# Optimization experiments

Hardware: AMD Instinct MI355X
Metric: run time of the kernel (lower is better)

The kernel has to match this reference:

```python
import jax, jax.numpy as jnp
import numpy as np

EPS = 1e-5

def conv1d(x, w, b, stride, pad):
    # x: [N, Cin, L], w: [Cout, Cin, K]
    out = jax.lax.conv_general_dilated(x, w, (stride,), [(pad, pad)], dimension_numbers=('NCH', 'OIH', 'NCH'))
    return out + b[None, :, None]

def bn_eval(x, g, b):
    # BatchNorm1d in eval mode with running_mean=0, running_var=1
    return x * (g / jnp.sqrt(1.0 + EPS))[None, :, None] + b[None, :, None]

def maxpool3(x):
    return jax.lax.reduce_window(x, -jnp.inf, jax.lax.max, (1, 1, 3), (1, 1, 3), 'VALID')

def layer_norm(x, g, b):
    m = x.mean(-1, keepdims=True)
    v = ((x - m) ** 2).mean(-1, keepdims=True)
    return (x - m) / jnp.sqrt(v + EPS) * g + b

def lstm_dir(x, w_ih, w_hh, b_ih, b_hh, reverse):
    # x: [B, S, I]; torch gate order i, f, g, o
    B = x.shape[0]; H = w_hh.shape[1]
    xs = jnp.einsum('bsi,gi->bsg', x, w_ih) + b_ih + b_hh
    if reverse:
        xs = xs[:, ::-1]
    def step(carry, xt):
        h, c = carry
        gates = xt + h @ w_hh.T
        i, f, g, o = jnp.split(gates, 4, axis=-1)
        c = jax.nn.sigmoid(f) * c + jax.nn.sigmoid(i) * jnp.tanh(g)
        h = jax.nn.sigmoid(o) * jnp.tanh(c)
        return (h, c), h
    init = (jnp.zeros((B, H), x.dtype), jnp.zeros((B, H), x.dtype))
    _, hs = jax.lax.scan(step, init, jnp.swapaxes(xs, 0, 1))
    hs = jnp.swapaxes(hs, 0, 1)
    return hs[:, ::-1] if reverse else hs

def setup_inputs() -> dict:
    key = jax.random.key(0)
    ks = iter(jax.random.split(key, 48))
    def rn(shape, s=0.05):
        return jax.random.normal(next(ks), shape, jnp.float32) * s
    B, S, C, T, F0, Hg, Hl, NC = 64, 20, 8, 3000, 64, 128, 256, 5
    return dict(
        x=jax.random.normal(next(ks), (B, S, C, T), jnp.float32),
        edge_index=jax.random.randint(next(ks), (2, 56), 0, C, jnp.int32),
        conv1_w=rn((16, 1, 7)), conv1_b=jnp.zeros(16), bn1_g=jnp.ones(16), bn1_b=jnp.zeros(16),
        conv2_w=rn((32, 16, 5)), conv2_b=jnp.zeros(32), bn2_g=jnp.ones(32), bn2_b=jnp.zeros(32),
        conv3_w=rn((F0, 32, 3)), conv3_b=jnp.zeros(F0), bn3_g=jnp.ones(F0), bn3_b=jnp.zeros(F0),
        gcn0_w=rn((Hg, F0)), gcn0_b=jnp.zeros(Hg),
        gcn1_w=rn((Hg, Hg)), gcn1_b=jnp.zeros(Hg),
        gnn_ln_g=jnp.ones(Hg), gnn_ln_b=jnp.zeros(Hg),
        w_ih_l0=rn((4 * Hl, Hg)), w_hh_l0=rn((4 * Hl, Hl)), b_ih_l0=jnp.zeros(4 * Hl), b_hh_l0=jnp.zeros(4 * Hl),
        w_ih_l0r=rn((4 * Hl, Hg)), w_hh_l0r=rn((4 * Hl, Hl)), b_ih_l0r=jnp.zeros(4 * Hl), b_hh_l0r=jnp.zeros(4 * Hl),
        w_ih_l1=rn((4 * Hl, 2 * Hl)), w_hh_l1=rn((4 * Hl, Hl)), b_ih_l1=jnp.zeros(4 * Hl), b_hh_l1=jnp.zeros(4 * Hl),
        w_ih_l1r=rn((4 * Hl, 2 * Hl)), w_hh_l1r=rn((4 * Hl, Hl)), b_ih_l1r=jnp.zeros(4 * Hl), b_hh_l1r=jnp.zeros(4 * Hl),
        lstm_ln_g=jnp.ones(2 * Hl), lstm_ln_b=jnp.zeros(2 * Hl),
        cls_w=rn((NC, 2 * Hl)), cls_b=jnp.zeros(NC),
    )

def reference(x, edge_index, conv1_w, conv1_b, bn1_g, bn1_b, conv2_w, conv2_b, bn2_g, bn2_b, conv3_w, conv3_b, bn3_g, bn3_b, gcn0_w, gcn0_b, gcn1_w, gcn1_b, gnn_ln_g, gnn_ln_b, w_ih_l0, w_hh_l0, b_ih_l0, b_hh_l0, w_ih_l0r, w_hh_l0r, b_ih_l0r, b_hh_l0r, w_ih_l1, w_hh_l1, b_ih_l1, b_hh_l1, w_ih_l1r, w_hh_l1r, b_ih_l1r, b_hh_l1r, lstm_ln_g, lstm_ln_b, cls_w, cls_b):
    B, S, C, T = x.shape
    # batched per-channel CNN over all B*S epochs at once (original: python double loop)
    h = x.reshape(B * S * C, 1, T)
    h = maxpool3(jax.nn.relu(bn_eval(conv1d(h, conv1_w, conv1_b, 2, 3), bn1_g, bn1_b)))
    h = maxpool3(jax.nn.relu(bn_eval(conv1d(h, conv2_w, conv2_b, 2, 2), bn2_g, bn2_b)))
    h = jax.nn.relu(bn_eval(conv1d(h, conv3_w, conv3_b, 1, 1), bn3_g, bn3_b))
    feats = h.mean(-1).reshape(B * S, C, -1)  # AdaptiveAvgPool1d(1) -> [BS, C, 64]
    # GCNConv normalized adjacency: D^-1/2 (A + I) D^-1/2, graph is tiny (C nodes) so dense is exact and efficient
    src, dst = edge_index[0], edge_index[1]
    A = jnp.zeros((C, C), x.dtype).at[dst, src].add(1.0) + jnp.eye(C, dtype=x.dtype)
    dinv = 1.0 / jnp.sqrt(A.sum(1))
    An = A * dinv[:, None] * dinv[None, :]
    g1 = jax.nn.relu(jnp.einsum('ij,bjf->bif', An, feats @ gcn0_w.T) + gcn0_b)  # dropout off (eval)
    g2 = jnp.einsum('ij,bjf->bif', An, g1 @ gcn1_w.T) + gcn1_b
    g2 = layer_norm(g2, gnn_ln_g, gnn_ln_b)
    emb = g2.mean(1).reshape(B, S, -1)  # mean over nodes -> [B, S, 128]
    l0 = jnp.concatenate([lstm_dir(emb, w_ih_l0, w_hh_l0, b_ih_l0, b_hh_l0, False),
                          lstm_dir(emb, w_ih_l0r, w_hh_l0r, b_ih_l0r, b_hh_l0r, True)], -1)
    l1 = jnp.concatenate([lstm_dir(l0, w_ih_l1, w_hh_l1, b_ih_l1, b_hh_l1, False),
                          lstm_dir(l0, w_ih_l1r, w_hh_l1r, b_ih_l1r, b_hh_l1r, True)], -1)
    out = layer_norm(l1, lstm_ln_g, lstm_ln_b)
    return out @ cls_w.T + cls_b  # [B, S, 5]
```

## Files before the change

kernel.cpp:

```cpp
#include <hip/hip_runtime.h>
#include <hip/hip_bf16.h>

#define DEVI __device__ __forceinline__

typedef _Float16 h2f16 __attribute__((ext_vector_type(2)));
typedef _Float16 f16x4 __attribute__((ext_vector_type(4)));
typedef _Float16 f16x8 __attribute__((ext_vector_type(8)));
typedef float    f32x4 __attribute__((ext_vector_type(4)));
union U4H { uint4 u; h2f16 h[4]; };
union F8  { f16x8 v8; f16x4 v4[2]; };

DEVI float sigf(float x){ return 1.f/(1.f + __expf(-x)); }
DEVI float tanh_f(float x){
  float ax = fabsf(x);
  float e = __expf(-2.f*ax);
  float t = (1.f - e)/(1.f + e);
  return copysignf(t, x);
}
DEVI h2f16 hmax2(h2f16 a, h2f16 b){
  h2f16 r; r[0] = a[0] > b[0] ? a[0] : b[0]; r[1] = a[1] > b[1] ? a[1] : b[1]; return r;
}

__global__ __launch_bounds__(256) void k_prep(
  const int* __restrict__ ei, float* __restrict__ An,
  const float* __restrict__ w2, const float* __restrict__ w3,
  const float* __restrict__ bg2, const float* __restrict__ bg3,
  _Float16* __restrict__ bw2f, _Float16* __restrict__ bw3f,
  const float* __restrict__ a0, const float* __restrict__ a1,
  const float* __restrict__ a2, const float* __restrict__ a3,
  const float* __restrict__ a4, const float* __restrict__ a5,
  _Float16* __restrict__ o0, _Float16* __restrict__ o1,
  _Float16* __restrict__ o2, _Float16* __restrict__ o3,
  _Float16* __restrict__ o4, _Float16* __restrict__ o5,
  const float* __restrict__ whh0, const float* __restrict__ whh0r,
  const float* __restrict__ whh1, const float* __restrict__ whh1r,
  h2f16* __restrict__ wt0f, h2f16* __restrict__ wt0r,
  h2f16* __restrict__ wt1f, h2f16* __restrict__ wt1r)
{
  const int bid = blockIdx.x, tid = threadIdx.x;
  if (bid == 0){
    __shared__ float A[64];
    __shared__ float dinv[8];
    if (tid<64) A[tid] = ((tid>>3)==(tid&7)) ? 1.f : 0.f;
    __syncthreads();
    if (tid==0){
      for (int e=0;e<56;e++){ int s=ei[e], d=ei[56+e]; A[d*8+s] += 1.f; }
    }
    __syncthreads();
    if (tid<8){ float s=0.f; for (int j=0;j<8;j++) s+=A[tid*8+j]; dinv[tid]=rsqrtf(s); }
    __syncthreads();
    if (tid<64) An[tid] = A[tid]*dinv[tid>>3]*dinv[tid&7];
    return;
  }
  if (bid <= 24){
    const int i = (bid-1)*256 + tid;
    const float rs = rsqrtf(1.f+1e-5f);
    if (i < 3072){
      const int j = i&7, m = (i>>3)&15, g = (i>>7)&3, nt = (i>>9)&1, s = i>>10;
      const int kk = 32*s + 8*g + j;
      const int k = kk >> 4, ic = kk & 15, oc = nt*16 + m;
      bw2f[i] = (_Float16)((k < 5 ? w2[oc*80 + ic*5 + k] : 0.f) * (bg2[oc]*rs));
    }
    if (i < 6144){
      const int j = i&7, m = (i>>3)&15, g = (i>>7)&3, wv = (i>>9)&3, s = i>>11;
      const int kk = 32*s + 8*g + j;
      const int k = kk >> 5, ic = kk & 31, oc = wv*16 + m;
      bw3f[i] = (_Float16)(w3[oc*96 + ic*3 + k] * (bg3[oc]*rs));
    }
    return;
  }
  if (bid <= 5240){
    const int i = (bid-25)*256 + tid;
    if      (i <  131072) o0[i] = (_Float16)a0[i];
    else if (i <  262144) o1[i-131072] = (_Float16)a1[i-131072];
    else if (i <  786432) o2[i-262144] = (_Float16)a2[i-262144];
    else if (i < 1310720) o3[i-786432] = (_Float16)a3[i-786432];
    else if (i < 1318912) o4[i-1310720] = (_Float16)a4[i-1310720];
    else if (i < 1335296) o5[i-1318912] = (_Float16)a5[i-1318912];
    return;
  }
  {
    __shared__ float tl[64][65];
    const int t = bid - 5241;
    const int which = t >> 6, tile = t & 63;
    const int tg = tile >> 2, tc = tile & 3;
    const float* in = (which==0) ? whh0 : (which==1) ? whh0r : (which==2) ? whh1 : whh1r;
    h2f16* outp    = (which==0) ? wt0f : (which==1) ? wt0r  : (which==2) ? wt1f : wt1r;
    #pragma unroll
    for (int p=0;p<16;p++){
      const int lin = p*256 + tid;
      const int r = lin >> 6, cc = lin & 63;
      tl[r][cc] = in[(tg*64 + r)*256 + tc*64 + cc];
    }
    __syncthreads();
    #pragma unroll
    for (int p=0;p<8;p++){
      const int lin = p*256 + tid;
      const int gl = lin & 63, jph = lin >> 6;
      h2f16 v;
      v[0] = (_Float16)tl[gl][2*jph];
      v[1] = (_Float16)tl[gl][2*jph+1];
      outp[(long)(tc*32 + jph)*1024 + tg*64 + gl] = v;
    }
  }
}

__global__ __launch_bounds__(512,8) void k_conv(
    const float* __restrict__ x,
    const float* __restrict__ w1g, const float* __restrict__ c1b,
    const float* __restrict__ bg1, const float* __restrict__ bb1,
    const _Float16* __restrict__ bw2f,
    const float* __restrict__ c2b, const float* __restrict__ bg2, const float* __restrict__ bb2,
    const _Float16* __restrict__ bw3f,
    const float* __restrict__ c3b, const float* __restrict__ bg3, const float* __restrict__ bb3,
    _Float16* __restrict__ feats)
{
  __shared__ __align__(16) unsigned char smb[38592];
  __shared__ h2f16 w1p[16][4];
  __shared__ float kb1o[16], kb2o[32], kb3o[64];
  __shared__ float redc[8][16];
  h2f16* sxh = reinterpret_cast<h2f16*>(smb + 20160);
  const int tid = threadIdx.x;
  const long sig = blockIdx.x;
  const float* xg = x + sig*3000;

  {
    const float4* xg4 = reinterpret_cast<const float4*>(xg);
    for (int i=tid; i<750; i+=512){
      float4 v = xg4[i];
      h2f16 p0; p0[0]=(_Float16)v.x; p0[1]=(_Float16)v.y;
      h2f16 p1; p1[0]=(_Float16)v.z; p1[1]=(_Float16)v.w;
      sxh[2*i+2] = p0; sxh[2*i+3] = p1;
    }
    if (tid<3){
      h2f16 z; z[0]=(_Float16)0.f; z[1]=(_Float16)0.f;
      sxh[tid<2 ? tid : 1502] = z;
    }
    if (tid<32){
      const int rr = tid>>3, cp = tid&7;
      const int row = (rr<2) ? rr : (500+rr);
      h2f16 z; z[0]=(_Float16)0.f; z[1]=(_Float16)0.f;
      *reinterpret_cast<h2f16*>(smb + row*40 + 4*cp) = z;
    }
    const float rs = rsqrtf(1.f+1e-5f);
    if (tid<64){
      const int c = tid>>2, j = tid&3;
      const float s = bg1[c]*rs;
      h2f16 p;
      if (j==0){ p[0]=(_Float16)0.f; p[1]=(_Float16)(w1g[c*7+0]*s); }
      else     { p[0]=(_Float16)(w1g[c*7+2*j-1]*s); p[1]=(_Float16)(w1g[c*7+2*j]*s); }
      w1p[c][j] = p;
    }
    if (tid<16) kb1o[tid] = c1b[tid]*(bg1[tid]*rs) + bb1[tid];
    if (tid<32) kb2o[tid] = c2b[tid]*(bg2[tid]*rs) + bb2[tid];
    if (tid<64) kb3o[tid] = c3b[tid]*(bg3[tid]*rs) + bb3[tid];
  }
  __syncthreads();

  {
    const int cp = tid & 7;
    h2f16 wpa[4], wpb[4];
    #pragma unroll
    for (int j=0;j<4;j++){ wpa[j] = w1p[2*cp][j]; wpb[j] = w1p[2*cp+1][j]; }
    const float oa = kb1o[2*cp], ob = kb1o[2*cp+1];
    for (int u = tid>>3; u<500; u+=64){
      h2f16 xq[6];
      #pragma unroll
      for (int r=0;r<6;r++) xq[r] = sxh[3*u + r];
      float a0=0.f,a1=0.f,a2=0.f,b0=0.f,b1=0.f,b2=0.f;
      #pragma unroll
      for (int j=0;j<4;j++){
        a0 = __builtin_amdgcn_fdot2(xq[j],   wpa[j], a0, false);
        a1 = __builtin_amdgcn_fdot2(xq[j+1], wpa[j], a1, false);
        a2 = __builtin_amdgcn_fdot2(xq[j+2], wpa[j], a2, false);
        b0 = __builtin_amdgcn_fdot2(xq[j],   wpb[j], b0, false);
        b1 = __builtin_amdgcn_fdot2(xq[j+1], wpb[j], b1, false);
        b2 = __builtin_amdgcn_fdot2(xq[j+2], wpb[j], b2, false);
      }
      const float ya = fmaxf(fmaxf(fmaxf(a0,a1),a2) + oa, 0.f);
      const float yb = fmaxf(fmaxf(fmaxf(b0,b1),b2) + ob, 0.f);
      h2f16 p; p[0]=(_Float16)ya; p[1]=(_Float16)yb;
      *reinterpret_cast<h2f16*>(smb + (u+2)*40 + 4*cp) = p;
    }
  }
  __syncthreads();

  const int wv = tid >> 6, lane = tid & 63;
  const int m = lane & 15, g = lane >> 4;

  {
    const int nt = wv & 1;
    f16x8 bf[3];
    #pragma unroll
    for (int s=0;s<3;s++)
      bf[s] = *reinterpret_cast<const f16x8*>(&bw2f[(((s*2+nt)*4+g)*16+m)*8]);
    const int oc = nt*16 + m;
    const float of = kb2o[oc];
    #pragma unroll
    for (int i=0;i<4;i++){
      const int mt = (wv>>1) + 4*i;
      const int trow = mt*16 + m;
      f32x4 acc = {0.f,0.f,0.f,0.f};
      #pragma unroll
      for (int s=0;s<3;s++){
        const int kk = 32*s + 8*g;
        const int k = kk >> 4;
        const int ab = 80*trow + 40*k + 16*(g&1);
        F8 a;
        a.v4[0] = *reinterpret_cast<const f16x4*>(smb + ab);
        a.v4[1] = *reinterpret_cast<const f16x4*>(smb + ab + 8);
        acc = __builtin_amdgcn_mfma_f32_16x16x32_f16(a.v8, bf[s], acc, 0,0,0);
      }
      #pragma unroll
      for (int r=0;r<4;r++){
        const int t = mt*16 + 4*g + r;
        const float z = fmaxf(acc[r] + of, 0.f);
        *reinterpret_cast<_Float16*>(smb + 20160 + t*72 + 2*oc) = (_Float16)z;
      }
    }
  }
  __syncthreads();

  {
    if (tid < 240){
      const int rr = tid >> 4, cc = tid & 15;
      const int row = (rr == 0) ? 0 : (83 + rr);
      h2f16 z; z[0]=(_Float16)0.f; z[1]=(_Float16)0.f;
      *reinterpret_cast<h2f16*>(smb + row*80 + 4*cc) = z;
    }
    for (int i=tid; i<1328; i+=512){
      const int u = i >> 4, cc = i & 15;
      h2f16 a = *reinterpret_cast<const h2f16*>(smb + 20160 + (3*u)*72 + 4*cc);
      h2f16 b = *reinterpret_cast<const h2f16*>(smb + 20160 + (3*u+1)*72 + 4*cc);
      h2f16 c = *reinterpret_cast<const h2f16*>(smb + 20160 + (3*u+2)*72 + 4*cc);
      *reinterpret_cast<h2f16*>(smb + (u+1)*80 + 4*cc) = hmax2(hmax2(a,b), c);
    }
  }
  __syncthreads();

  {
    const int nt = wv & 3;
    f16x8 bf[3];
    #pragma unroll
    for (int s=0;s<3;s++)
      bf[s] = *reinterpret_cast<const f16x8*>(&bw3f[(((s*4+nt)*4+g)*16+m)*8]);
    const int oc = nt*16 + m;
    const float of = kb3o[oc];
    float macc = 0.f;
    #pragma unroll
    for (int q=0;q<3;q++){
      const int mt = (wv>>2) + 2*q;
      const int trow = mt*16 + m;
      f32x4 acc = {0.f,0.f,0.f,0.f};
      #pragma unroll
      for (int s=0;s<3;s++){
        f16x8 af = *reinterpret_cast<const f16x8*>(smb + (trow + s)*80 + 16*g);
        acc = __builtin_amdgcn_mfma_f32_16x16x32_f16(af, bf[s], acc, 0,0,0);
      }
      #pragma unroll
      for (int r=0;r<4;r++){
        const int t = mt*16 + 4*g + r;
        if (t < 83) macc += fmaxf(acc[r] + of, 0.f);
      }
    }
    macc += __shfl_xor(macc, 16);
    macc += __shfl_xor(macc, 32);
    if (lane < 16) redc[wv][m] = macc;
  }
  __syncthreads();
  if (tid < 64)
    feats[sig*64 + tid] = (_Float16)((redc[tid>>4][tid&15] + redc[(tid>>4)+4][tid&15]) * (1.f/83.f));
}

__global__ __launch_bounds__(256) void k_gcn(
  const _Float16* __restrict__ feats, const _Float16* __restrict__ W0,
  const _Float16* __restrict__ W1,
  const float* __restrict__ An, const float* __restrict__ b0,
  const float* __restrict__ b1, const float* __restrict__ lng,
  const float* __restrict__ lnb, _Float16* __restrict__ emb)
{
  __shared__ __align__(16) unsigned char lds[66304];
  __shared__ float ans[64];
  unsigned char* Xs  = lds;
  unsigned char* Ws0 = lds + 4608;
  float*         Cs  = reinterpret_cast<float*>(lds + 13824);
  unsigned char* W1s = lds + 13824;
  unsigned char* g1h = lds + 48896;
  const int tid = threadIdx.x;
  const int m0 = blockIdx.x*64;
  const int wv = tid>>6, lane = tid&63, m = lane&15, g = lane>>4;
  const int sr = tid>>2, sq = tid&3;
  if (tid<64) ans[tid] = An[tid];
  {
    f32x4 acc[8] = {};
    for (int k0=0; k0<64; k0+=32){
      uint4 xa  = *reinterpret_cast<const uint4*>(feats + (long)(m0+sr)*64 + k0 + sq*8);
      uint4 wa0 = *reinterpret_cast<const uint4*>(W0 + (long)sr*64 + k0 + sq*8);
      uint4 wa1 = *reinterpret_cast<const uint4*>(W0 + (long)(sr+64)*64 + k0 + sq*8);
      __syncthreads();
      *reinterpret_cast<uint4*>(Xs + sr*72 + sq*16) = xa;
      *reinterpret_cast<uint4*>(Ws0 + sr*72 + sq*16) = wa0;
      *reinterpret_cast<uint4*>(Ws0 + (sr+64)*72 + sq*16) = wa1;
      __syncthreads();
      f16x8 af = *reinterpret_cast<const f16x8*>(Xs + (wv*16+m)*72 + g*16);
      #pragma unroll
      for (int nt=0;nt<8;nt++){
        f16x8 bf = *reinterpret_cast<const f16x8*>(Ws0 + (nt*16+m)*72 + g*16);
        acc[nt] = __builtin_amdgcn_mfma_f32_16x16x32_f16(af, bf, acc[nt], 0,0,0);
      }
    }
    __syncthreads();
    #pragma unroll
    for (int nt=0;nt<8;nt++)
      #pragma unroll
      for (int r=0;r<4;r++)
        Cs[(wv*16 + g*4 + r)*132 + nt*16 + m] = acc[nt][r];
  }
  __syncthreads();
  for (int idx=tid; idx<1024; idx+=256){
    const int gg = idx>>7, j = idx&127;
    float t[8];
    #pragma unroll
    for (int c=0;c<8;c++) t[c] = Cs[(gg*8+c)*132 + j];
    const float bj = b0[j];
    #pragma unroll
    for (int i=0;i<8;i++){
      float s = bj;
      #pragma unroll
      for (int c=0;c<8;c++) s += ans[i*8+c]*t[c];
      *reinterpret_cast<_Float16*>(g1h + (gg*8+i)*272 + j*2) = (_Float16)fmaxf(s, 0.f);
    }
  }
  __syncthreads();
  for (int i2=tid; i2<2048; i2+=256){
    const int row = i2>>4, q = i2&15;
    *reinterpret_cast<uint4*>(W1s + row*272 + q*16) =
        *reinterpret_cast<const uint4*>(W1 + (long)row*128 + q*8);
  }
  __syncthreads();
  {
    f32x4 acc2[8] = {};
    #pragma unroll
    for (int kc=0;kc<4;kc++){
      f16x8 af = *reinterpret_cast<const f16x8*>(g1h + (wv*16+m)*272 + kc*64 + g*16);
      #pragma unroll
      for (int nt=0;nt<8;nt++){
        f16x8 bf = *reinterpret_cast<const f16x8*>(W1s + (nt*16+m)*272 + kc*64 + g*16);
        acc2[nt] = __builtin_amdgcn_mfma_f32_16x16x32_f16(af, bf, acc2[nt], 0,0,0);
      }
    }
    __syncthreads();
    #pragma unroll
    for (int nt=0;nt<8;nt++)
      #pragma unroll
      for (int r=0;r<4;r++)
        Cs[(wv*16 + g*4 + r)*132 + nt*16 + m] = acc2[nt][r];
  }
  __syncthreads();
  {
    const int s = tid>>5, l = tid&31;
    float g2v[8][4];
    #pragma unroll
    for (int jj=0;jj<4;jj++){
      const int j = l + jj*32;
      float t[8];
      #pragma unroll
      for (int c=0;c<8;c++) t[c] = Cs[(s*8+c)*132 + j];
      const float bj = b1[j];
      #pragma unroll
      for (int i=0;i<8;i++){
        float v = bj;
        #pragma unroll
        for (int c=0;c<8;c++) v += ans[i*8+c]*t[c];
        g2v[i][jj] = v;
      }
    }
    float mi[8], ri[8];
    #pragma unroll
    for (int i=0;i<8;i++){
      float sm=0.f, sq2=0.f;
      #pragma unroll
      for (int jj=0;jj<4;jj++){ sm += g2v[i][jj]; sq2 += g2v[i][jj]*g2v[i][jj]; }
      #pragma unroll
      for (int off=16; off>=1; off>>=1){ sm += __shfl_xor(sm, off); sq2 += __shfl_xor(sq2, off); }
      const float mu = sm*(1.f/128.f);
      mi[i] = mu;
      ri[i] = rsqrtf(sq2*(1.f/128.f) - mu*mu + 1e-5f);
    }
    #pragma unroll
    for (int jj=0;jj<4;jj++){
      const int j = l + jj*32;
      float a = 0.f;
      #pragma unroll
      for (int i=0;i<8;i++) a += (g2v[i][jj]-mi[i])*ri[i];
      emb[(long)(blockIdx.x*8 + s)*128 + j] = (_Float16)(lng[j]*a*0.125f + lnb[j]);
    }
  }
}

__global__ __launch_bounds__(512) void k_gemm_mf2(
  const _Float16* __restrict__ X,
  const _Float16* __restrict__ Wa, const _Float16* __restrict__ Wb,
  const float* __restrict__ b1a, const float* __restrict__ b2a,
  const float* __restrict__ b1b, const float* __restrict__ b2b,
  _Float16* __restrict__ C, int K)
{
  __shared__ __align__(16) unsigned char lds[13824];
  unsigned char* Xs = lds;
  unsigned char* Ws = lds + 9216;
  const int z = blockIdx.z;
  const _Float16* W = z ? Wb : Wa;
  const float* b1 = z ? b1b : b1a;
  const float* b2 = z ? b2b : b2a;
  _Float16* Cz = C + (z ? 1024 : 0);
  const int tid = threadIdx.x;
  const int m0 = blockIdx.y*128, n0 = blockIdx.x*64;
  const int wv = tid>>6, lane = tid&63, m = lane&15, g = lane>>4;
  const int sr = tid>>2, sq = tid&3;
  f32x4 acc[4] = {{0.f,0.f,0.f,0.f},{0.f,0.f,0.f,0.f},{0.f,0.f,0.f,0.f},{0.f,0.f,0.f,0.f}};
  for (int k0=0; k0<K; k0+=32){
    uint4 xa = *reinterpret_cast<const uint4*>(X + (long)(m0+sr)*K + k0 + sq*8);
    uint4 wa = make_uint4(0,0,0,0);
    if (tid < 256)
      wa = *reinterpret_cast<const uint4*>(W + (long)(n0+sr)*K + k0 + sq*8);
    __syncthreads();
    *reinterpret_cast<uint4*>(Xs + sr*72 + sq*16) = xa;
    if (tid < 256) *reinterpret_cast<uint4*>(Ws + sr*72 + sq*16) = wa;
    __syncthreads();
    f16x8 af = *reinterpret_cast<const f16x8*>(Xs + (wv*16+m)*72 + g*16);
    #pragma unroll
    for (int nt=0;nt<4;nt++){
      f16x8 bf = *reinterpret_cast<const f16x8*>(Ws + (nt*16+m)*72 + g*16);
      acc[nt] = __builtin_amdgcn_mfma_f32_16x16x32_f16(af, bf, acc[nt], 0,0,0);
    }
  }
  #pragma unroll
  for (int nt=0;nt<4;nt++){
    const int col = n0 + nt*16 + m;
    float bias = b1[col] + b2[col];
    #pragma unroll
    for (int r=0;r<4;r++)
      Cz[(long)(m0 + wv*16 + g*4 + r)*2048 + col] = (_Float16)(acc[nt][r] + bias);
  }
}

__global__ __launch_bounds__(1024) void k_lstm(
    const _Float16* __restrict__ xs,
    const h2f16* __restrict__ wtf,
    const h2f16* __restrict__ wtr,
    float* __restrict__ outf,
    _Float16* __restrict__ outh)
{
  const int S = 20;
  const int b = blockIdx.x >> 1, dir = blockIdx.x & 1;
  const h2f16* wt = dir ? wtr : wtf;
  __shared__ float part[4][1024];
  __shared__ _Float16 hsh[256];
  __shared__ __align__(16) unsigned char wlds[131072];
  const int tid = threadIdx.x;
  const int jg = tid >> 8, r = tid & 255, grow = r*4;
  uint4 wreg[16];
  #pragma unroll
  for (int jp=0;jp<16;jp++)
    wreg[jp] = *reinterpret_cast<const uint4*>(
        reinterpret_cast<const unsigned int*>(wt + (long)(jg*32+jp)*1024 + grow));
  {
    const uint4* wsrc = reinterpret_cast<const uint4*>(wt);
    uint4* wdst = reinterpret_cast<uint4*>(wlds);
    for (int i=tid; i<8192; i+=1024){
      const int src = (i < 4096) ? (4096 + i) : (12288 + (i - 4096));
      wdst[i] = wsrc[src];
    }
  }
  if (tid < 256) hsh[tid] = (_Float16)0.f;
  float cc = 0.f;
  __syncthreads();
  const h2f16* hp2 = reinterpret_cast<const h2f16*>(hsh);
  for (int st=0; st<S; ++st){
    const int t = dir ? (S-1-st) : st;
    float a0=0.f,a1=0.f,a2=0.f,a3=0.f;
    #pragma unroll
    for (int jp=0; jp<16; ++jp){
      const h2f16 hv = hp2[jg*32 + jp];
      U4H w; w.u = wreg[jp];
      a0 = __builtin_amdgcn_fdot2(hv, w.h[0], a0, false);
      a1 = __builtin_amdgcn_fdot2(hv, w.h[1], a1, false);
      a2 = __builtin_amdgcn_fdot2(hv, w.h[2], a2, false);
      a3 = __builtin_amdgcn_fdot2(hv, w.h[3], a3, false);
    }
    if (jg < 2){
      #pragma unroll 8
      for (int jp=16; jp<32; ++jp){
        const h2f16 hv = hp2[jg*32 + jp];
        U4H w; w.u = *reinterpret_cast<const uint4*>(
            wlds + (long)(jg*16 + (jp-16))*4096 + grow*4);
        a0 = __builtin_amdgcn_fdot2(hv, w.h[0], a0, false);
        a1 = __builtin_amdgcn_fdot2(hv, w.h[1], a1, false);
        a2 = __builtin_amdgcn_fdot2(hv, w.h[2], a2, false);
        a3 = __builtin_amdgcn_fdot2(hv, w.h[3], a3, false);
      }
    } else {
      #pragma unroll 8
      for (int jp=16; jp<32; ++jp){
        const h2f16 hv = hp2[jg*32 + jp];
        U4H w; w.u = *reinterpret_cast<const uint4*>(
            reinterpret_cast<const unsigned int*>(wt + (long)(jg*32+jp)*1024 + grow));
        a0 = __builtin_amdgcn_fdot2(hv, w.h[0], a0, false);
        a1 = __builtin_amdgcn_fdot2(hv, w.h[1], a1, false);
        a2 = __builtin_amdgcn_fdot2(hv, w.h[2], a2, false);
        a3 = __builtin_amdgcn_fdot2(hv, w.h[3], a3, false);
      }
    }
    *reinterpret_cast<float4*>(&part[jg][grow]) = make_float4(a0,a1,a2,a3);
    __syncthreads();
    if (tid < 256){
      const _Float16* xrow = xs + ((long)b*S + t)*2048 + dir*1024;
      float g0 = (float)xrow[tid]
               + (part[0][tid]      + part[1][tid])      + (part[2][tid]      + part[3][tid]);
      float g1 = (float)xrow[256+tid]
               + (part[0][256+tid]  + part[1][256+tid])  + (part[2][256+tid]  + part[3][256+tid]);
      float g2 = (float)xrow[512+tid]
               + (part[0][512+tid]  + part[1][512+tid])  + (part[2][512+tid]  + part[3][512+tid]);
      float g3 = (float)xrow[768+tid]
               + (part[0][768+tid]  + part[1][768+tid])  + (part[2][768+tid]  + part[3][768+tid]);
      cc = sigf(g1)*cc + sigf(g0)*tanh_f(g2);
      const float h = sigf(g3)*tanh_f(cc);
      hsh[tid] = (_Float16)h;
      const long o = ((long)b*S + t)*512 + dir*256 + tid;
      if (outf) outf[o] = h;
      if (outh) outh[o] = (_Float16)h;
    }
    __syncthreads();
  }
}

__global__ __launch_bounds__(128) void k_lncls(
  const float* __restrict__ in, const float* __restrict__ g,
  const float* __restrict__ b, const float* __restrict__ cw,
  const float* __restrict__ cb, float* __restrict__ out)
{
  const int row = blockIdx.x, tid = threadIdx.x;
  __shared__ float sred[4];
  __shared__ float cred[2][5];
  float4 v = *reinterpret_cast<const float4*>(in + (long)row*512 + tid*4);
  float s  = v.x+v.y+v.z+v.w;
  float sq = v.x*v.x+v.y*v.y+v.z*v.z+v.w*v.w;
  #pragma unroll
  for (int off=32; off>=1; off>>=1){ s += __shfl_xor(s, off); sq += __shfl_xor(sq, off); }
  const int wv = tid>>6;
  if ((tid&63)==0){ sred[wv*2]=s; sred[wv*2+1]=sq; }
  __syncthreads();
  const float S = sred[0]+sred[2], SQ = sred[1]+sred[3];
  const float m = S*(1.f/512.f);
  const float rstd = rsqrtf(SQ*(1.f/512.f) - m*m + 1e-5f);
  float4 gg = *reinterpret_cast<const float4*>(g + tid*4);
  float4 bb = *reinterpret_cast<const float4*>(b + tid*4);
  const float n0 = (v.x-m)*rstd*gg.x + bb.x;
  const float n1 = (v.y-m)*rstd*gg.y + bb.y;
  const float n2 = (v.z-m)*rstd*gg.z + bb.z;
  const float n3 = (v.w-m)*rstd*gg.w + bb.w;
  #pragma unroll
  for (int nc=0; nc<5; ++nc){
    float4 w = *reinterpret_cast<const float4*>(cw + nc*512 + tid*4);
    float p = n0*w.x + n1*w.y + n2*w.z + n3*w.w;
    #pragma unroll
    for (int off=32; off>=1; off>>=1) p += __shfl_xor(p, off);
    if ((tid&63)==0) cred[wv][nc] = p;
  }
  __syncthreads();
  if (tid < 5) out[(long)row*5 + tid] = cred[0][tid] + cred[1][tid] + cb[tid];
}

extern "C" void kernel_launch(void* const* d_in, const int* in_sizes, int n_in,
                              void* d_out, int out_size, void* d_ws, size_t ws_size,
                              hipStream_t stream)
{
  const float* x     = (const float*)d_in[0];
  const int*   ei    = (const int*)d_in[1];
  const float* w1    = (const float*)d_in[2];
  const float* c1b   = (const float*)d_in[3];
  const float* bg1   = (const float*)d_in[4];
  const float* bb1   = (const float*)d_in[5];
  const float* w2    = (const float*)d_in[6];
  const float* c2b   = (const float*)d_in[7];
  const float* bg2   = (const float*)d_in[8];
  const float* bb2   = (const float*)d_in[9];
  const float* w3    = (const float*)d_in[10];
  const float* c3b   = (const float*)d_in[11];
  const float* bg3   = (const float*)d_in[12];
  const float* bb3   = (const float*)d_in[13];
  const float* gcn0w = (const float*)d_in[14];
  const float* gcn0b = (const float*)d_in[15];
  const float* gcn1w = (const float*)d_in[16];
  const float* gcn1b = (const float*)d_in[17];
  const float* lng   = (const float*)d_in[18];
  const float* lnb   = (const float*)d_in[19];
  const float* wih0  = (const float*)d_in[20];
  const float* whh0  = (const float*)d_in[21];
  const float* bih0  = (const float*)d_in[22];
  const float* bhh0  = (const float*)d_in[23];
  const float* wih0r = (const float*)d_in[24];
  const float* whh0r = (const float*)d_in[25];
  const float* bih0r = (const float*)d_in[26];
  const float* bhh0r = (const float*)d_in[27];
  const float* wih1  = (const float*)d_in[28];
  const float* whh1  = (const float*)d_in[29];
  const float* bih1  = (const float*)d_in[30];
  const float* bhh1  = (const float*)d_in[31];
  const float* wih1r = (const float*)d_in[32];
  const float* whh1r = (const float*)d_in[33];
  const float* bih1r = (const float*)d_in[34];
  const float* bhh1r = (const float*)d_in[35];
  const float* lstmg = (const float*)d_in[36];
  const float* lstmb = (const float*)d_in[37];
  const float* clsw  = (const float*)d_in[38];
  const float* clsb  = (const float*)d_in[39];
  float* ws  = (float*)d_ws;
  float* out = (float*)d_out;

  float*    An      = ws + 0;
  _Float16* bw2f    = (_Float16*)(ws + 64);
  _Float16* bw3f    = (_Float16*)(ws + 1600);
  _Float16* feats16 = (_Float16*)(ws + 4672);
  _Float16* g1b16   = (_Float16*)(ws + 332352);
  _Float16* emb16   = (_Float16*)(ws + 987712);
  _Float16* l0h     = (_Float16*)(ws + 1069632);
  _Float16* w0f     = (_Float16*)(ws + 1397312);
  _Float16* w0rf    = (_Float16*)(ws + 1462848);
  _Float16* w1f     = (_Float16*)(ws + 1528384);
  _Float16* w1rf    = (_Float16*)(ws + 1790528);
  _Float16* gw0f    = (_Float16*)(ws + 2052672);
  _Float16* gw1f    = (_Float16*)(ws + 2056768);
  h2f16*    wt0f    = (h2f16*)(ws + 2064960);
  h2f16*    wt0r    = (h2f16*)(ws + 2196032);
  h2f16*    wt1f    = (h2f16*)(ws + 2327104);
  h2f16*    wt1r    = (h2f16*)(ws + 2458176);
  float*    l1f     = ws + 2589248;
  _Float16* xsh     = (_Float16*)(ws + 3244608);

  k_prep<<<5497, 256, 0, stream>>>(ei, An, w2, w3, bg2, bg3, bw2f, bw3f,
                                   wih0, wih0r, wih1, wih1r, gcn0w, gcn1w,
                                   w0f, w0rf, w1f, w1rf, gw0f, gw1f,
                                   whh0, whh0r, whh1, whh1r,
                                   wt0f, wt0r, wt1f, wt1r);
  k_conv<<<10240, 512, 0, stream>>>(x, w1,c1b,bg1,bb1, bw2f,c2b,bg2,bb2,
                                    bw3f,c3b,bg3,bb3, feats16);

  k_gcn<<<160, 256, 0, stream>>>(feats16, gw0f, gw1f, An, gcn0b, gcn1b,
                                 lng, lnb, emb16);

  k_gemm_mf2<<<dim3(16, 10, 2), 512, 0, stream>>>(emb16, w0f, w0rf,
      bih0, bhh0, bih0r, bhh0r, xsh, 128);
  k_lstm<<<128, 1024, 0, stream>>>(xsh, wt0f, wt0r, nullptr, l0h);

  k_gemm_mf2<<<dim3(16, 10, 2), 512, 0, stream>>>(l0h, w1f, w1rf,
      bih1, bhh1, bih1r, bhh1r, xsh, 512);
  k_lstm<<<128, 1024, 0, stream>>>(xsh, wt1f, wt1r, l1f, nullptr);

  k_lncls<<<1280, 128, 0, stream>>>(l1f, lstmg, lstmb, clsw, clsb, out);
}
```

Measured before the change: 296.5 us.

## Move conv1 stage to MFMA with per-wave smem staging; vectorize weight conversion

```diff
diff --git a/kernel.cpp b/kernel.cpp
--- a/kernel.cpp
+++ b/kernel.cpp
@@ -20,9 +20,17 @@
 DEVI h2f16 hmax2(h2f16 a, h2f16 b){
   h2f16 r; r[0] = a[0] > b[0] ? a[0] : b[0]; r[1] = a[1] > b[1] ? a[1] : b[1]; return r;
 }
+DEVI f16x4 hmax4(f16x4 a, f16x4 b){
+  f16x4 r;
+  #pragma unroll
+  for (int i=0;i<4;i++) r[i] = a[i] > b[i] ? a[i] : b[i];
+  return r;
+}
 
 __global__ __launch_bounds__(256) void k_prep(
   const int* __restrict__ ei, float* __restrict__ An,
+  const float* __restrict__ w1, const float* __restrict__ bg1,
+  _Float16* __restrict__ bw1f,
   const float* __restrict__ w2, const float* __restrict__ w3,
   const float* __restrict__ bg2, const float* __restrict__ bg3,
   _Float16* __restrict__ bw2f, _Float16* __restrict__ bw3f,
@@ -55,6 +63,15 @@
   if (bid <= 24){
     const int i = (bid-1)*256 + tid;
     const float rs = rsqrtf(1.f+1e-5f);
+    if (i < 512){
+      const int j = i&7, mm = (i>>3)&15, gg = i>>7;
+      float v = 0.f;
+      if (gg==0){
+        if (j<4)      v = w1[mm*7 + 2*j]     * (bg1[mm]*rs);
+        else if (j<7) v = w1[mm*7 + 2*j - 7] * (bg1[mm]*rs);
+      }
+      bw1f[i] = (_Float16)v;
+    }
     if (i < 3072){
       const int j = i&7, m = (i>>3)&15, g = (i>>7)&3, nt = (i>>9)&1, s = i>>10;
       const int kk = 32*s + 8*g + j;
@@ -69,19 +86,24 @@
     }
     return;
   }
-  if (bid <= 5240){
-    const int i = (bid-25)*256 + tid;
-    if      (i <  131072) o0[i] = (_Float16)a0[i];
-    else if (i <  262144) o1[i-131072] = (_Float16)a1[i-131072];
-    else if (i <  786432) o2[i-262144] = (_Float16)a2[i-262144];
-    else if (i < 1310720) o3[i-786432] = (_Float16)a3[i-786432];
-    else if (i < 1318912) o4[i-1310720] = (_Float16)a4[i-1310720];
-    else if (i < 1335296) o5[i-1318912] = (_Float16)a5[i-1318912];
+  if (bid <= 1328){
+    const int q4 = (bid-25)*256 + tid;
+    const float* s; _Float16* d; long off;
+    if      (q4 <  32768){ s=a0; d=o0; off=(long)q4*4; }
+    else if (q4 <  65536){ s=a1; d=o1; off=(long)(q4-32768)*4; }
+    else if (q4 < 196608){ s=a2; d=o2; off=(long)(q4-65536)*4; }
+    else if (q4 < 327680){ s=a3; d=o3; off=(long)(q4-196608)*4; }
+    else if (q4 < 329728){ s=a4; d=o4; off=(long)(q4-327680)*4; }
+    else                 { s=a5; d=o5; off=(long)(q4-329728)*4; }
+    float4 v = *reinterpret_cast<const float4*>(s + off);
+    f16x4 h;
+    h[0]=(_Float16)v.x; h[1]=(_Float16)v.y; h[2]=(_Float16)v.z; h[3]=(_Float16)v.w;
+    *reinterpret_cast<f16x4*>(d + off) = h;
     return;
   }
   {
     __shared__ float tl[64][65];
-    const int t = bid - 5241;
+    const int t = bid - 1329;
     const int which = t >> 6, tile = t & 63;
     const int tg = tile >> 2, tc = tile & 3;
     const float* in = (which==0) ? whh0 : (which==1) ? whh0r : (which==2) ? whh1 : whh1r;
@@ -107,17 +129,17 @@
 
 __global__ __launch_bounds__(512,8) void k_conv(
     const float* __restrict__ x,
-    const float* __restrict__ w1g, const float* __restrict__ c1b,
-    const float* __restrict__ bg1, const float* __restrict__ bb1,
+    const _Float16* __restrict__ bw1f,
+    const float* __restrict__ c1b, const float* __restrict__ bg1, const float* __restrict__ bb1,
     const _Float16* __restrict__ bw2f,
     const float* __restrict__ c2b, const float* __restrict__ bg2, const float* __restrict__ bb2,
     const _Float16* __restrict__ bw3f,
     const float* __restrict__ c3b, const float* __restrict__ bg3, const float* __restrict__ bb3,
     _Float16* __restrict__ feats)
 {
-  __shared__ __align__(16) unsigned char smb[38592];
-  __shared__ h2f16 w1p[16][4];
-  __shared__ float kb1o[16], kb2o[32], kb3o[64];
+  __shared__ __align__(16) unsigned char smb[39488];
+  __shared__ __align__(8) _Float16 kb1oh[16];
+  __shared__ float kb2o[32], kb3o[64];
   __shared__ float redc[8][16];
   h2f16* sxh = reinterpret_cast<h2f16*>(smb + 20160);
   const int tid = threadIdx.x;
@@ -143,50 +165,69 @@
       *reinterpret_cast<h2f16*>(smb + row*40 + 4*cp) = z;
     }
     const float rs = rsqrtf(1.f+1e-5f);
-    if (tid<64){
-      const int c = tid>>2, j = tid&3;
-      const float s = bg1[c]*rs;
-      h2f16 p;
-      if (j==0){ p[0]=(_Float16)0.f; p[1]=(_Float16)(w1g[c*7+0]*s); }
-      else     { p[0]=(_Float16)(w1g[c*7+2*j-1]*s); p[1]=(_Float16)(w1g[c*7+2*j]*s); }
-      w1p[c][j] = p;
-    }
-    if (tid<16) kb1o[tid] = c1b[tid]*(bg1[tid]*rs) + bb1[tid];
+    if (tid<16) kb1oh[tid] = (_Float16)(c1b[tid]*(bg1[tid]*rs) + bb1[tid]);
     if (tid<32) kb2o[tid] = c2b[tid]*(bg2[tid]*rs) + bb2[tid];
     if (tid<64) kb3o[tid] = c3b[tid]*(bg3[tid]*rs) + bb3[tid];
   }
   __syncthreads();
 
-  {
-    const int cp = tid & 7;
-    h2f16 wpa[4], wpb[4];
-    #pragma unroll
-    for (int j=0;j<4;j++){ wpa[j] = w1p[2*cp][j]; wpb[j] = w1p[2*cp+1][j]; }
-    const float oa = kb1o[2*cp], ob = kb1o[2*cp+1];
-    for (int u = tid>>3; u<500; u+=64){
-      h2f16 xq[6];
-      #pragma unroll
-      for (int r=0;r<6;r++) xq[r] = sxh[3*u + r];
-      float a0=0.f,a1=0.f,a2=0.f,b0=0.f,b1=0.f,b2=0.f;
-      #pragma unroll
-      for (int j=0;j<4;j++){
-        a0 = __builtin_amdgcn_fdot2(xq[j],   wpa[j], a0, false);
-        a1 = __builtin_amdgcn_fdot2(xq[j+1], wpa[j], a1, false);
-        a2 = __builtin_amdgcn_fdot2(xq[j+2], wpa[j], a2, false);
-        b0 = __builtin_amdgcn_fdot2(xq[j],   wpb[j], b0, false);
-        b1 = __builtin_amdgcn_fdot2(xq[j+1], wpb[j], b1, false);
-        b2 = __builtin_amdgcn_fdot2(xq[j+2], wpb[j], b2, false);
-      }
-      const float ya = fmaxf(fmaxf(fmaxf(a0,a1),a2) + oa, 0.f);
-      const float yb = fmaxf(fmaxf(fmaxf(b0,b1),b2) + ob, 0.f);
-      h2f16 p; p[0]=(_Float16)ya; p[1]=(_Float16)yb;
-      *reinterpret_cast<h2f16*>(smb + (u+2)*40 + 4*cp) = p;
-    }
-  }
-  __syncthreads();
-
   const int wv = tid >> 6, lane = tid & 63;
   const int m = lane & 15, g = lane >> 4;
+
+  {
+    unsigned char* wb = smb + 26176 + wv*1664;
+    const unsigned int* sx32 = reinterpret_cast<const unsigned int*>(smb + 20160);
+    for (int i=lane; i<104; i+=64)
+      *reinterpret_cast<uint4*>(wb + i*16) = make_uint4(0,0,0,0);
+    f16x8 bf1 = *reinterpret_cast<const f16x8*>(&bw1f[(g*16+m)*8]);
+    f16x4 offq = *reinterpret_cast<const f16x4*>(&kb1oh[(lane&3)*4]);
+    f16x4 zero4; zero4[0]=zero4[1]=zero4[2]=zero4[3]=(_Float16)0.f;
+    for (int ch = wv; ch < 32; ch += 8){
+      if (lane < 48){
+        const int trow = ch*48 + lane;
+        if (trow < 1500){
+          unsigned int u0=sx32[trow], u1=sx32[trow+1], u2=sx32[trow+2], u3=sx32[trow+3];
+          uint4 o;
+          o.x = (u1 & 0xffff0000u) | (u0 >> 16);
+          o.y = (u3 & 0xffff0000u) | (u2 >> 16);
+          o.z = (u2 << 16) | (u1 & 0xffffu);
+          o.w = u3 & 0xffffu;
+          *reinterpret_cast<uint4*>(wb + lane*16) = o;
+        }
+      }
+      f32x4 acc0, acc1, acc2;
+      {
+        f32x4 z = {0.f,0.f,0.f,0.f};
+        f16x8 af0 = *reinterpret_cast<const f16x8*>(wb + (0*16+m)*16 + g*16);
+        f16x8 af1 = *reinterpret_cast<const f16x8*>(wb + (1*16+m)*16 + g*16);
+        f16x8 af2 = *reinterpret_cast<const f16x8*>(wb + (2*16+m)*16 + g*16);
+        acc0 = __builtin_amdgcn_mfma_f32_16x16x32_f16(af0, bf1, z, 0,0,0);
+        acc1 = __builtin_amdgcn_mfma_f32_16x16x32_f16(af1, bf1, z, 0,0,0);
+        acc2 = __builtin_amdgcn_mfma_f32_16x16x32_f16(af2, bf1, z, 0,0,0);
+      }
+      #pragma unroll
+      for (int r=0;r<4;r++){
+        *reinterpret_cast<_Float16*>(wb + (0*16+4*g+r)*32 + m*2) = (_Float16)acc0[r];
+        *reinterpret_cast<_Float16*>(wb + (1*16+4*g+r)*32 + m*2) = (_Float16)acc1[r];
+        *reinterpret_cast<_Float16*>(wb + (2*16+4*g+r)*32 + m*2) = (_Float16)acc2[r];
+      }
+      {
+        const int ul = lane>>2, cq = lane&3;
+        const int ug = ch*16 + ul;
+        if (ug < 500){
+          f16x4 r0 = *reinterpret_cast<const f16x4*>(wb + (3*ul)*32 + cq*8);
+          f16x4 r1 = *reinterpret_cast<const f16x4*>(wb + (3*ul+1)*32 + cq*8);
+          f16x4 r2 = *reinterpret_cast<const f16x4*>(wb + (3*ul+2)*32 + cq*8);
+          f16x4 y = hmax4(hmax4(r0,r1),r2);
+          #pragma unroll
+          for (int i2=0;i2<4;i2++) y[i2] = y[i2] + offq[i2];
+          y = hmax4(y, zero4);
+          *reinterpret_cast<f16x4*>(smb + (ug+2)*40 + cq*8) = y;
+        }
+      }
+    }
+  }
+  __syncthreads();
 
   {
     const int nt = wv & 1;
@@ -622,7 +663,6 @@
   _Float16* bw2f    = (_Float16*)(ws + 64);
   _Float16* bw3f    = (_Float16*)(ws + 1600);
   _Float16* feats16 = (_Float16*)(ws + 4672);
-  _Float16* g1b16   = (_Float16*)(ws + 332352);
   _Float16* emb16   = (_Float16*)(ws + 987712);
   _Float16* l0h     = (_Float16*)(ws + 1069632);
   _Float16* w0f     = (_Float16*)(ws + 1397312);
@@ -637,14 +677,17 @@
   h2f16*    wt1r    = (h2f16*)(ws + 2458176);
   float*    l1f     = ws + 2589248;
   _Float16* xsh     = (_Float16*)(ws + 3244608);
-
-  k_prep<<<5497, 256, 0, stream>>>(ei, An, w2, w3, bg2, bg3, bw2f, bw3f,
+  _Float16* bw1f    = (_Float16*)(ws + 4555328);
+
+  k_prep<<<1585, 256, 0, stream>>>(ei, An, w1, bg1, bw1f,
+                                   w2, w3, bg2, bg3, bw2f, bw3f,
                                    wih0, wih0r, wih1, wih1r, gcn0w, gcn1w,
                                    w0f, w0rf, w1f, w1rf, gw0f, gw1f,
                                    whh0, whh0r, whh1, whh1r,
                                    wt0f, wt0r, wt1f, wt1r);
-  k_conv<<<10240, 512, 0, stream>>>(x, w1,c1b,bg1,bb1, bw2f,c2b,bg2,bb2,
-                                    bw3f,c3b,bg3,bb3, feats16);
+  k_conv<<<10240, 512, 0, stream>>>(x, bw1f, c1b, bg1, bb1,
+                                    bw2f, c2b, bg2, bb2,
+                                    bw3f, c3b, bg3, bb3, feats16);
 
   k_gcn<<<160, 256, 0, stream>>>(feats16, gw0f, gw1f, An, gcn0b, gcn1b,
                                  lng, lnb, emb16);
```

Measured after the change: 312.1 us. 5.3% more time.
